# Optimization experiments

Measured on AMD Instinct MI355X. Metric: run time of the kernel, lower is better.

## Reference

```python
import jax, jax.numpy as jnp
import numpy as np

P = 0.5  # dropout fraction (init kwarg p)


def setup_inputs() -> dict:
    key = jax.random.key(0)
    # positive weights (e.g. post-softmax attention), shape [B, M, N]
    w = jax.random.uniform(key, (8192, 1, 4096), dtype=jnp.float32, minval=1e-4, maxval=1.0)
    return {"w": w}


def reference(w) -> jnp.ndarray:
    # Drop the bottom int(N*P) entries along dim 2 (per row), then renormalize
    # the surviving entries with a softmax over them; dropped entries stay 0.
    B, M, N = w.shape
    k = int(N * P)  # number of smallest entries zeroed per row
    if k == 0:
        return w
    order = jnp.argsort(w, axis=2)          # ascending order indices
    ranks = jnp.argsort(order, axis=2)      # rank of each element in its row
    keep = ranks >= k                        # True for the top (N-k) entries
    neg = jnp.finfo(w.dtype).min
    logits = jnp.where(keep, w, neg)
    m = jnp.max(logits, axis=2, keepdims=True)
    e = jnp.where(keep, jnp.exp(logits - m), 0.0)
    return e / jnp.sum(e, axis=2, keepdims=True)
```

## Files before the change

kernel.cpp:

```cpp
#include <hip/hip_runtime.h>
#include <stdint.h>

constexpr int N     = 4096;
constexpr int KSEL  = 2048;
constexpr int BLOCK = 256;
constexpr int NW    = BLOCK / 64;
constexpr int EPT   = N / BLOCK;
constexpr int RPB   = 2;
constexpr int NB    = 256;
constexpr int CAP   = 128;
constexpr float P1  = 0.45f;
constexpr float P2  = 0.55f;
constexpr float BSCALE = 2560.0f;

__global__ __launch_bounds__(BLOCK, 4)
void wdrop_kernel(const float* __restrict__ w, float* __restrict__ out) {
    const int t = threadIdx.x, wid = t >> 6, lane = t & 63;
    const uint64_t row0 = (uint64_t)blockIdx.x * RPB;

    __shared__ int      hist[RPB][NB];
    __shared__ uint32_t redu[RPB][NW];
    __shared__ int      redi[RPB][NW];
    __shared__ float    redf[RPB][NW];
    __shared__ int      scanw[RPB][NW];
    __shared__ int      selb[RPB], selc[RPB];
    __shared__ int      cn[RPB];
    __shared__ uint32_t cb[RPB][CAP];
    __shared__ int      ci[RPB][CAP];
    __shared__ uint32_t thrT[RPB], thrI[RPB];

    uint32_t v[RPB][EPT];
    {
        const uint4* wf0 = (const uint4*)(w + row0 * N);
        const uint4* wf1 = (const uint4*)(w + (row0 + 1) * N);
        uint4 u0[EPT / 4], u1[EPT / 4];
#pragma unroll
        for (int j = 0; j < EPT / 4; ++j) u0[j] = wf0[j * BLOCK + t];
#pragma unroll
        for (int j = 0; j < EPT / 4; ++j) u1[j] = wf1[j * BLOCK + t];
#pragma unroll
        for (int j = 0; j < EPT / 4; ++j) {
            v[0][j*4+0]=u0[j].x; v[0][j*4+1]=u0[j].y; v[0][j*4+2]=u0[j].z; v[0][j*4+3]=u0[j].w;
            v[1][j*4+0]=u1[j].x; v[1][j*4+1]=u1[j].y; v[1][j*4+2]=u1[j].z; v[1][j*4+3]=u1[j].w;
        }
    }
    hist[0][t] = 0; hist[1][t] = 0;
    if (t < RPB) cn[t] = 0;

#pragma unroll
    for (int r = 0; r < RPB; ++r) {
        uint32_t mx = v[r][0];
        int clo = 0, chi = 0;
#pragma unroll
        for (int e = 0; e < EPT; ++e) {
            mx = max(mx, v[r][e]);
            const float f = __uint_as_float(v[r][e]);
            clo += (f < P1); chi += (f < P2);
        }
        int pk = (clo << 16) | chi;
#pragma unroll
        for (int off = 32; off > 0; off >>= 1) {
            mx = max(mx, (uint32_t)__shfl_xor((int)mx, off, 64));
            pk += __shfl_xor(pk, off, 64);
        }
        if (lane == 0) { redu[r][wid] = mx; redi[r][wid] = pk; }
    }
    __syncthreads();

    uint32_t mxb[RPB]; int jrank[RPB]; bool fast[RPB];
#pragma unroll
    for (int r = 0; r < RPB; ++r) {
        uint32_t m = redu[r][0]; int pk = redi[r][0];
#pragma unroll
        for (int i = 1; i < NW; ++i) { m = max(m, redu[r][i]); pk += redi[r][i]; }
        const int clo = pk >> 16, chi = pk & 0xFFFF;
        mxb[r] = m;
        fast[r]  = (clo < KSEL) && (chi >= KSEL);
        jrank[r] = KSEL - clo;
    }

#pragma unroll
    for (int r = 0; r < RPB; ++r) {
        if (fast[r]) {
#pragma unroll
            for (int e = 0; e < EPT; ++e) {
                const float f = __uint_as_float(v[r][e]);
                if (f >= P1 && f < P2) {
                    const int bk = min((int)((f - P1) * BSCALE), NB - 1);
                    atomicAdd(&hist[r][bk], 1);
                }
            }
        }
    }
    __syncthreads();

    const int h0 = hist[0][t], h1 = hist[1][t];
    int s0 = h0, s1 = h1;
#pragma unroll
    for (int off = 1; off < 64; off <<= 1) {
        const int u0 = __shfl_up(s0, off, 64);
        const int u1 = __shfl_up(s1, off, 64);
        if (lane >= off) { s0 += u0; s1 += u1; }
    }
    if (lane == 63) { scanw[0][wid] = s0; scanw[1][wid] = s1; }
    __syncthreads();
    int wb0 = 0, wb1 = 0;
#pragma unroll
    for (int i = 0; i < NW; ++i)
        if (i < wid) { wb0 += scanw[0][i]; wb1 += scanw[1][i]; }
    const int inc0 = s0 + wb0, exc0 = inc0 - h0;
    const int inc1 = s1 + wb1, exc1 = inc1 - h1;
    if (fast[0] && exc0 < jrank[0] && jrank[0] <= inc0) { selb[0] = t; selc[0] = exc0; }
    if (fast[1] && exc1 < jrank[1] && jrank[1] <= inc1) { selb[1] = t; selc[1] = exc1; }
    __syncthreads();

#pragma unroll
    for (int r = 0; r < RPB; ++r) {
        if (fast[r]) {
            const int bs = selb[r];
#pragma unroll
            for (int e = 0; e < EPT; ++e) {
                const float f = __uint_as_float(v[r][e]);
                if (f >= P1 && f < P2 && min((int)((f - P1) * BSCALE), NB - 1) == bs) {
                    const int slot = atomicAdd(&cn[r], 1);
                    if (slot < CAP) {
                        cb[r][slot] = v[r][e];
                        ci[r][slot] = ((e >> 2) * BLOCK + t) * 4 + (e & 3);
                    }
                }
            }
        }
    }
    __syncthreads();
#pragma unroll
    for (int r = 0; r < RPB; ++r) fast[r] = fast[r] && (cn[r] <= CAP);

#pragma unroll
    for (int r = 0; r < RPB; ++r) {
        if (fast[r] && t < cn[r]) {
            const uint32_t myb = cb[r][t]; const int myi = ci[r][t];
            int rank = 0;
            for (int q = 0; q < cn[r]; ++q)
                rank += (cb[r][q] < myb) || (cb[r][q] == myb && ci[r][q] < myi);
            if (rank == jrank[r] - selc[r] - 1) { thrT[r] = myb; thrI[r] = (uint32_t)myi; }
        }
    }
    __syncthreads();

    for (int r = 0; r < RPB; ++r) {
        if (!fast[r]) {
            uint32_t blo = 0u, bhi = 0x7f7fffffu;
            while (blo < bhi) {
                const uint32_t mid = blo + ((bhi - blo) >> 1);
                int c = 0;
#pragma unroll
                for (int e = 0; e < EPT; ++e) c += __popcll(__ballot(v[r][e] <= mid));
                __syncthreads();
                if (lane == 0) redi[r][wid] = c;
                __syncthreads();
                int tot = 0;
#pragma unroll
                for (int i = 0; i < NW; ++i) tot += redi[r][i];
                if (tot >= KSEL) bhi = mid; else blo = mid + 1;
            }
            const uint32_t T = blo;
            int c = 0;
#pragma unroll
            for (int e = 0; e < EPT; ++e) c += __popcll(__ballot(v[r][e] < T));
            __syncthreads();
            if (lane == 0) redi[r][wid] = c;
            __syncthreads();
            int clt = 0;
#pragma unroll
            for (int i = 0; i < NW; ++i) clt += redi[r][i];
            const int need = KSEL - clt;
            int ilo = 0, ihi = N - 1;
            while (ilo < ihi) {
                const int imid = (ilo + ihi) >> 1;
                int cc = 0;
#pragma unroll
                for (int e = 0; e < EPT; ++e) {
                    const int idx = ((e >> 2) * BLOCK + t) * 4 + (e & 3);
                    cc += __popcll(__ballot(v[r][e] == T && idx <= imid));
                }
                __syncthreads();
                if (lane == 0) redi[r][wid] = cc;
                __syncthreads();
                int tot = 0;
#pragma unroll
                for (int i = 0; i < NW; ++i) tot += redi[r][i];
                if (tot >= need) ihi = imid; else ilo = imid + 1;
            }
            if (t == 0) { thrT[r] = T; thrI[r] = (uint32_t)ilo; }
            __syncthreads();
        }
    }

    float s[RPB];
#pragma unroll
    for (int r = 0; r < RPB; ++r) {
        const uint32_t T = thrT[r]; const int ti = (int)thrI[r];
        const float m = __uint_as_float(mxb[r]);
        float acc = 0.0f;
#pragma unroll
        for (int e = 0; e < EPT; ++e) {
            const int idx = ((e >> 2) * BLOCK + t) * 4 + (e & 3);
            const bool keep = (v[r][e] > T) || (v[r][e] == T && idx > ti);
            const float ev = keep ? __expf(__uint_as_float(v[r][e]) - m) : 0.0f;
            v[r][e] = __float_as_uint(ev);
            acc += ev;
        }
#pragma unroll
        for (int off = 32; off > 0; off >>= 1) acc += __shfl_xor(acc, off, 64);
        if (lane == 0) redf[r][wid] = acc;
        s[r] = 0.0f;
    }
    __syncthreads();
#pragma unroll
    for (int r = 0; r < RPB; ++r) {
#pragma unroll
        for (int i = 0; i < NW; ++i) s[r] += redf[r][i];
        s[r] = 1.0f / s[r];
    }
#pragma unroll
    for (int r = 0; r < RPB; ++r) {
        uint4* of = (uint4*)(out + (row0 + r) * N);
#pragma unroll
        for (int j = 0; j < EPT / 4; ++j) {
            float4 o;
            o.x = __uint_as_float(v[r][j*4+0]) * s[r];
            o.y = __uint_as_float(v[r][j*4+1]) * s[r];
            o.z = __uint_as_float(v[r][j*4+2]) * s[r];
            o.w = __uint_as_float(v[r][j*4+3]) * s[r];
            ((float4*)of)[j * BLOCK + t] = o;
        }
    }
}

extern "C" void kernel_launch(void* const* d_in, const int* in_sizes, int n_in,
                              void* d_out, int out_size, void* d_ws, size_t ws_size,
                              hipStream_t stream) {
    const float* w = (const float*)d_in[0];
    float* out = (float*)d_out;
    const int rows = in_sizes[0] / N;
    wdrop_kernel<<<rows / RPB, BLOCK, 0, stream>>>(w, out);
}
```

Measured before the change: 232.6 us.

## Process rows sequentially per block with register prefetch of the next row

Each block now handles four rows one at a time. While the current row is being processed, the next row's data is loaded into registers, so global load latency overlaps with the selection and softmax work. Shared-memory scratch is shrunk to a single row's worth, and the occupancy hint in launch bounds is raised. In exchange, the grid has fewer blocks, and the per-row barriers now run one after another inside each block, which could leave CUs underused.

```diff
diff --git a/kernel.cpp b/kernel.cpp
--- a/kernel.cpp
+++ b/kernel.cpp
@@ -6,55 +6,55 @@
 constexpr int BLOCK = 256;
 constexpr int NW    = BLOCK / 64;
 constexpr int EPT   = N / BLOCK;
-constexpr int RPB   = 2;
+constexpr int RPB   = 4;
 constexpr int NB    = 256;
 constexpr int CAP   = 128;
 constexpr float P1  = 0.45f;
 constexpr float P2  = 0.55f;
 constexpr float BSCALE = 2560.0f;
 
-__global__ __launch_bounds__(BLOCK, 4)
+__global__ __launch_bounds__(BLOCK, 8)
 void wdrop_kernel(const float* __restrict__ w, float* __restrict__ out) {
     const int t = threadIdx.x, wid = t >> 6, lane = t & 63;
     const uint64_t row0 = (uint64_t)blockIdx.x * RPB;
 
-    __shared__ int      hist[RPB][NB];
-    __shared__ uint32_t redu[RPB][NW];
-    __shared__ int      redi[RPB][NW];
-    __shared__ float    redf[RPB][NW];
-    __shared__ int      scanw[RPB][NW];
-    __shared__ int      selb[RPB], selc[RPB];
-    __shared__ int      cn[RPB];
-    __shared__ uint32_t cb[RPB][CAP];
-    __shared__ int      ci[RPB][CAP];
-    __shared__ uint32_t thrT[RPB], thrI[RPB];
-
-    uint32_t v[RPB][EPT];
+    __shared__ int      hist[NB];
+    __shared__ uint32_t redu[NW];
+    __shared__ int      redi[NW];
+    __shared__ float    redf[NW];
+    __shared__ int      scanw[NW];
+    __shared__ int      selb, selc, cn;
+    __shared__ uint32_t cbv[CAP];
+    __shared__ int      civ[CAP];
+    __shared__ uint32_t thrT, thrI;
+
+    uint4 nb[EPT / 4];
     {
-        const uint4* wf0 = (const uint4*)(w + row0 * N);
-        const uint4* wf1 = (const uint4*)(w + (row0 + 1) * N);
-        uint4 u0[EPT / 4], u1[EPT / 4];
-#pragma unroll
-        for (int j = 0; j < EPT / 4; ++j) u0[j] = wf0[j * BLOCK + t];
-#pragma unroll
-        for (int j = 0; j < EPT / 4; ++j) u1[j] = wf1[j * BLOCK + t];
+        const uint4* wf = (const uint4*)(w + row0 * N);
+#pragma unroll
+        for (int j = 0; j < EPT / 4; ++j) nb[j] = wf[j * BLOCK + t];
+    }
+
+    for (int r = 0; r < RPB; ++r) {
+        uint32_t v[EPT];
 #pragma unroll
         for (int j = 0; j < EPT / 4; ++j) {
-            v[0][j*4+0]=u0[j].x; v[0][j*4+1]=u0[j].y; v[0][j*4+2]=u0[j].z; v[0][j*4+3]=u0[j].w;
-            v[1][j*4+0]=u1[j].x; v[1][j*4+1]=u1[j].y; v[1][j*4+2]=u1[j].z; v[1][j*4+3]=u1[j].w;
-        }
-    }
-    hist[0][t] = 0; hist[1][t] = 0;
-    if (t < RPB) cn[t] = 0;
-
-#pragma unroll
-    for (int r = 0; r < RPB; ++r) {
-        uint32_t mx = v[r][0];
+            v[4*j+0] = nb[j].x; v[4*j+1] = nb[j].y; v[4*j+2] = nb[j].z; v[4*j+3] = nb[j].w;
+        }
+        if (r + 1 < RPB) {
+            const uint4* wn = (const uint4*)(w + (row0 + r + 1) * N);
+#pragma unroll
+            for (int j = 0; j < EPT / 4; ++j) nb[j] = wn[j * BLOCK + t];
+        }
+        hist[t] = 0;
+        if (t == 0) cn = 0;
+
+        uint32_t mx = v[0];
         int clo = 0, chi = 0;
 #pragma unroll
         for (int e = 0; e < EPT; ++e) {
-            mx = max(mx, v[r][e]);
-            const float f = __uint_as_float(v[r][e]);
+            mx = max(mx, v[e]);
+            const float f = __uint_as_float(v[e]);
             clo += (f < P1); chi += (f < P2);
         }
         int pk = (clo << 16) | chi;
@@ -63,116 +63,88 @@
             mx = max(mx, (uint32_t)__shfl_xor((int)mx, off, 64));
             pk += __shfl_xor(pk, off, 64);
         }
-        if (lane == 0) { redu[r][wid] = mx; redi[r][wid] = pk; }
-    }
-    __syncthreads();
-
-    uint32_t mxb[RPB]; int jrank[RPB]; bool fast[RPB];
-#pragma unroll
-    for (int r = 0; r < RPB; ++r) {
-        uint32_t m = redu[r][0]; int pk = redi[r][0];
-#pragma unroll
-        for (int i = 1; i < NW; ++i) { m = max(m, redu[r][i]); pk += redi[r][i]; }
-        const int clo = pk >> 16, chi = pk & 0xFFFF;
-        mxb[r] = m;
-        fast[r]  = (clo < KSEL) && (chi >= KSEL);
-        jrank[r] = KSEL - clo;
-    }
-
-#pragma unroll
-    for (int r = 0; r < RPB; ++r) {
-        if (fast[r]) {
+        if (lane == 0) { redu[wid] = mx; redi[wid] = pk; }
+        __syncthreads();
+        uint32_t mxb = redu[0]; int pks = redi[0];
+#pragma unroll
+        for (int i = 1; i < NW; ++i) { mxb = max(mxb, redu[i]); pks += redi[i]; }
+        const int clo_b = pks >> 16, chi_b = pks & 0xFFFF;
+        bool fast = (clo_b < KSEL) && (chi_b >= KSEL);
+        const int jrank = KSEL - clo_b;
+
+        if (fast) {
 #pragma unroll
             for (int e = 0; e < EPT; ++e) {
-                const float f = __uint_as_float(v[r][e]);
-                if (f >= P1 && f < P2) {
-                    const int bk = min((int)((f - P1) * BSCALE), NB - 1);
-                    atomicAdd(&hist[r][bk], 1);
-                }
-            }
-        }
-    }
-    __syncthreads();
-
-    const int h0 = hist[0][t], h1 = hist[1][t];
-    int s0 = h0, s1 = h1;
-#pragma unroll
-    for (int off = 1; off < 64; off <<= 1) {
-        const int u0 = __shfl_up(s0, off, 64);
-        const int u1 = __shfl_up(s1, off, 64);
-        if (lane >= off) { s0 += u0; s1 += u1; }
-    }
-    if (lane == 63) { scanw[0][wid] = s0; scanw[1][wid] = s1; }
-    __syncthreads();
-    int wb0 = 0, wb1 = 0;
-#pragma unroll
-    for (int i = 0; i < NW; ++i)
-        if (i < wid) { wb0 += scanw[0][i]; wb1 += scanw[1][i]; }
-    const int inc0 = s0 + wb0, exc0 = inc0 - h0;
-    const int inc1 = s1 + wb1, exc1 = inc1 - h1;
-    if (fast[0] && exc0 < jrank[0] && jrank[0] <= inc0) { selb[0] = t; selc[0] = exc0; }
-    if (fast[1] && exc1 < jrank[1] && jrank[1] <= inc1) { selb[1] = t; selc[1] = exc1; }
-    __syncthreads();
-
-#pragma unroll
-    for (int r = 0; r < RPB; ++r) {
-        if (fast[r]) {
-            const int bs = selb[r];
+                const float f = __uint_as_float(v[e]);
+                if (f >= P1 && f < P2)
+                    atomicAdd(&hist[min((int)((f - P1) * BSCALE), NB - 1)], 1);
+            }
+            __syncthreads();
+            const int h = hist[t];
+            int sc = h;
+#pragma unroll
+            for (int off = 1; off < 64; off <<= 1) {
+                const int u = __shfl_up(sc, off, 64);
+                if (lane >= off) sc += u;
+            }
+            if (lane == 63) scanw[wid] = sc;
+            __syncthreads();
+            int wb = 0;
+#pragma unroll
+            for (int i = 0; i < NW; ++i) if (i < wid) wb += scanw[i];
+            const int inc = sc + wb, exc = inc - h;
+            if (exc < jrank && jrank <= inc) { selb = t; selc = exc; }
+            __syncthreads();
+            const int bs = selb;
 #pragma unroll
             for (int e = 0; e < EPT; ++e) {
-                const float f = __uint_as_float(v[r][e]);
+                const float f = __uint_as_float(v[e]);
                 if (f >= P1 && f < P2 && min((int)((f - P1) * BSCALE), NB - 1) == bs) {
-                    const int slot = atomicAdd(&cn[r], 1);
+                    const int slot = atomicAdd(&cn, 1);
                     if (slot < CAP) {
-                        cb[r][slot] = v[r][e];
-                        ci[r][slot] = ((e >> 2) * BLOCK + t) * 4 + (e & 3);
+                        cbv[slot] = v[e];
+                        civ[slot] = ((e >> 2) * BLOCK + t) * 4 + (e & 3);
                     }
                 }
             }
-        }
-    }
-    __syncthreads();
-#pragma unroll
-    for (int r = 0; r < RPB; ++r) fast[r] = fast[r] && (cn[r] <= CAP);
-
-#pragma unroll
-    for (int r = 0; r < RPB; ++r) {
-        if (fast[r] && t < cn[r]) {
-            const uint32_t myb = cb[r][t]; const int myi = ci[r][t];
-            int rank = 0;
-            for (int q = 0; q < cn[r]; ++q)
-                rank += (cb[r][q] < myb) || (cb[r][q] == myb && ci[r][q] < myi);
-            if (rank == jrank[r] - selc[r] - 1) { thrT[r] = myb; thrI[r] = (uint32_t)myi; }
-        }
-    }
-    __syncthreads();
-
-    for (int r = 0; r < RPB; ++r) {
-        if (!fast[r]) {
+            __syncthreads();
+            if (cn <= CAP) {
+                if (t < cn) {
+                    const uint32_t myb = cbv[t]; const int myi = civ[t];
+                    int rank = 0;
+                    for (int q = 0; q < cn; ++q)
+                        rank += (cbv[q] < myb) || (cbv[q] == myb && civ[q] < myi);
+                    if (rank == jrank - selc - 1) { thrT = myb; thrI = (uint32_t)myi; }
+                }
+            } else fast = false;
+            __syncthreads();
+        }
+
+        if (!fast) {
             uint32_t blo = 0u, bhi = 0x7f7fffffu;
             while (blo < bhi) {
                 const uint32_t mid = blo + ((bhi - blo) >> 1);
                 int c = 0;
 #pragma unroll
-                for (int e = 0; e < EPT; ++e) c += __popcll(__ballot(v[r][e] <= mid));
-                __syncthreads();
-                if (lane == 0) redi[r][wid] = c;
+                for (int e = 0; e < EPT; ++e) c += __popcll(__ballot(v[e] <= mid));
+                __syncthreads();
+                if (lane == 0) redi[wid] = c;
                 __syncthreads();
                 int tot = 0;
 #pragma unroll
-                for (int i = 0; i < NW; ++i) tot += redi[r][i];
+                for (int i = 0; i < NW; ++i) tot += redi[i];
                 if (tot >= KSEL) bhi = mid; else blo = mid + 1;
             }
             const uint32_t T = blo;
             int c = 0;
 #pragma unroll
-            for (int e = 0; e < EPT; ++e) c += __popcll(__ballot(v[r][e] < T));
-            __syncthreads();
-            if (lane == 0) redi[r][wid] = c;
+            for (int e = 0; e < EPT; ++e) c += __popcll(__ballot(v[e] < T));
+            __syncthreads();
+            if (lane == 0) redi[wid] = c;
             __syncthreads();
             int clt = 0;
 #pragma unroll
-            for (int i = 0; i < NW; ++i) clt += redi[r][i];
+            for (int i = 0; i < NW; ++i) clt += redi[i];
             const int need = KSEL - clt;
             int ilo = 0, ihi = N - 1;
             while (ilo < ihi) {
@@ -181,57 +153,47 @@
 #pragma unroll
                 for (int e = 0; e < EPT; ++e) {
                     const int idx = ((e >> 2) * BLOCK + t) * 4 + (e & 3);
-                    cc += __popcll(__ballot(v[r][e] == T && idx <= imid));
+                    cc += __popcll(__ballot(v[e] == T && idx <= imid));
                 }
                 __syncthreads();
-                if (lane == 0) redi[r][wid] = cc;
+                if (lane == 0) redi[wid] = cc;
                 __syncthreads();
                 int tot = 0;
 #pragma unroll
-                for (int i = 0; i < NW; ++i) tot += redi[r][i];
+                for (int i = 0; i < NW; ++i) tot += redi[i];
                 if (tot >= need) ihi = imid; else ilo = imid + 1;
             }
-            if (t == 0) { thrT[r] = T; thrI[r] = (uint32_t)ilo; }
-            __syncthreads();
-        }
-    }
-
-    float s[RPB];
-#pragma unroll
-    for (int r = 0; r < RPB; ++r) {
-        const uint32_t T = thrT[r]; const int ti = (int)thrI[r];
-        const float m = __uint_as_float(mxb[r]);
+            if (t == 0) { thrT = T; thrI = (uint32_t)ilo; }
+            __syncthreads();
+        }
+
+        const uint32_t T = thrT; const int ti = (int)thrI;
+        const float m = __uint_as_float(mxb);
         float acc = 0.0f;
 #pragma unroll
         for (int e = 0; e < EPT; ++e) {
             const int idx = ((e >> 2) * BLOCK + t) * 4 + (e & 3);
-            const bool keep = (v[r][e] > T) || (v[r][e] == T && idx > ti);
-            const float ev = keep ? __expf(__uint_as_float(v[r][e]) - m) : 0.0f;
-            v[r][e] = __float_as_uint(ev);
+            const bool keep = (v[e] > T) || (v[e] == T && idx > ti);
+            const float ev = keep ? __expf(__uint_as_float(v[e]) - m) : 0.0f;
+            v[e] = __float_as_uint(ev);
             acc += ev;
         }
 #pragma unroll
         for (int off = 32; off > 0; off >>= 1) acc += __shfl_xor(acc, off, 64);
-        if (lane == 0) redf[r][wid] = acc;
-        s[r] = 0.0f;
-    }
-    __syncthreads();
-#pragma unroll
-    for (int r = 0; r < RPB; ++r) {
-#pragma unroll
-        for (int i = 0; i < NW; ++i) s[r] += redf[r][i];
-        s[r] = 1.0f / s[r];
-    }
-#pragma unroll
-    for (int r = 0; r < RPB; ++r) {
+        if (lane == 0) redf[wid] = acc;
+        __syncthreads();
+        float tot = 0.0f;
+#pragma unroll
+        for (int i = 0; i < NW; ++i) tot += redf[i];
+        const float inv = 1.0f / tot;
         uint4* of = (uint4*)(out + (row0 + r) * N);
 #pragma unroll
         for (int j = 0; j < EPT / 4; ++j) {
             float4 o;
-            o.x = __uint_as_float(v[r][j*4+0]) * s[r];
-            o.y = __uint_as_float(v[r][j*4+1]) * s[r];
-            o.z = __uint_as_float(v[r][j*4+2]) * s[r];
-            o.w = __uint_as_float(v[r][j*4+3]) * s[r];
+            o.x = __uint_as_float(v[4*j+0]) * inv;
+            o.y = __uint_as_float(v[4*j+1]) * inv;
+            o.z = __uint_as_float(v[4*j+2]) * inv;
+            o.w = __uint_as_float(v[4*j+3]) * inv;
             ((float4*)of)[j * BLOCK + t] = o;
         }
     }
```

After: 263.1 us. 13.1% more time.
